# Kernel optimization log

Measured on AMD Instinct MI355X. Metric: run time of the kernel, lower is better.

The kernel has to match this reference:

```python
import jax, jax.numpy as jnp
import numpy as np

P, Q = 4, 16            # mlp_quad_last_shape
N, D_IN, H = 100000, 3, 256
N_QUAD = 128


def setup_inputs() -> dict:
    key = jax.random.key(0)
    ks = jax.random.split(key, 20)
    sc = lambda fan: 1.0 / np.sqrt(fan)
    inp = {}
    inp["input"] = jax.random.normal(ks[0], (N, D_IN), jnp.float32)
    inp["eq_param"] = jax.random.uniform(ks[1], (1,), jnp.float32)
    for i in range(5):
        inp[f"quad_x{i}"] = jax.random.uniform(ks[2 + i], (N_QUAD, 1), jnp.float32)
    # mlp_x params: Linear(3->256) -> tanh -> Linear(256->1024=P^5)
    inp["Wx1"] = jax.random.normal(ks[7], (D_IN, H), jnp.float32) * sc(D_IN)
    inp["bx1"] = jnp.zeros((H,), jnp.float32)
    inp["Wx2"] = jax.random.normal(ks[8], (H, P ** 5), jnp.float32) * sc(H)
    inp["bx2"] = jnp.zeros((P ** 5,), jnp.float32)
    # per-axis quad MLPs: Linear(1 -> P*Q)
    for i in range(5):
        inp[f"Wq{i}"] = jax.random.normal(ks[9 + i], (1, P * Q), jnp.float32) * sc(1)
        inp[f"bq{i}"] = jnp.zeros((P * Q,), jnp.float32)
    return inp


def reference(input, eq_param, quad_x0, quad_x1, quad_x2, quad_x3, quad_x4,
              Wx1, bx1, Wx2, bx2,
              Wq0, bq0, Wq1, bq1, Wq2, bq2, Wq3, bq3, Wq4, bq4):
    # lhs = mlp_x(input): [N, P^5]
    lhs = jnp.tanh(input @ Wx1 + bx1) @ Wx2 + bx2

    quads = (quad_x0, quad_x1, quad_x2, quad_x3, quad_x4)
    Ws = (Wq0, Wq1, Wq2, Wq3, Wq4)
    bs = (bq0, bq1, bq2, bq3, bq4)

    # Each factor: out_quad_i = y_i * (quad_x_i @ Wq_i + bq_i), reshape [n_i, P, Q].
    # The original einsum 'abx,cdx,efx,lmx,wvx->abcdeflmwv' followed by movedims,
    # reshape and sum over the merged n-axes is a multilinear map, so summing
    # each factor over its n_i axis FIRST gives the identical rhs tensor
    # (sum commutes with the outer product), avoiding the 10-D intermediate.
    ss = []
    for qx, W, b in zip(quads, Ws, bs):
        y = jnp.exp(-jnp.sum(qx * qx, axis=-1, keepdims=True) * eq_param[0])  # r_func weight [n_i,1]
        oq = (y * (qx @ W + b)).reshape(-1, P, Q)  # [n_i, P, Q]
        ss.append(jnp.sum(oq, axis=0))             # [P, Q]
    s0, s1, s2, s3, s4 = ss
    # rhs[b,d,f,m,v] = sum_x s0[b,x] s1[d,x] s2[f,x] s3[m,x] s4[v,x]  -> flatten to [P^5]
    rhs = jnp.einsum('bx,dx,fx,mx,vx->bdfmv', s0, s1, s2, s3, s4).reshape(-1)
    return lhs @ rhs  # [N]
```

## Files before the change

kernel.cpp:

```cpp
#include <hip/hip_runtime.h>

#define PP 4
#define QQ 16
#define NQ 128
#define HH 256
#define P5 1024

__device__ __forceinline__ float block_sum256(float v, float* red, int t) {
#pragma unroll
  for (int o = 32; o > 0; o >>= 1) v += __shfl_down(v, o, 64);
  if ((t & 63) == 0) red[t >> 6] = v;
  __syncthreads();
  float r = red[0] + red[1] + red[2] + red[3];
  __syncthreads();
  return r;
}

__global__ __launch_bounds__(256) void prep_kernel(
    const float* __restrict__ eq,
    const float* __restrict__ q0, const float* __restrict__ q1,
    const float* __restrict__ q2, const float* __restrict__ q3,
    const float* __restrict__ q4,
    const float* __restrict__ Wx1, const float* __restrict__ bx1,
    const float* __restrict__ Wx2, const float* __restrict__ bx2,
    const float* __restrict__ Wq0, const float* __restrict__ bq0,
    const float* __restrict__ Wq1, const float* __restrict__ bq1,
    const float* __restrict__ Wq2, const float* __restrict__ bq2,
    const float* __restrict__ Wq3, const float* __restrict__ bq3,
    const float* __restrict__ Wq4, const float* __restrict__ bq4,
    float* __restrict__ ws) {
  __shared__ float red[4];
  __shared__ float sS[5][64];
  __shared__ float sRhs[P5];

  const int t = threadIdx.x;
  const int hb = blockIdx.x;
  const float eqv = eq[0];

  const float* qs[5]  = {q0, q1, q2, q3, q4};
  const float* Wqs[5] = {Wq0, Wq1, Wq2, Wq3, Wq4};
  const float* bqs[5] = {bq0, bq1, bq2, bq3, bq4};

  float A[5], B[5];
#pragma unroll
  for (int i = 0; i < 5; ++i) {
    float a = 0.f, b = 0.f;
    if (t < NQ) {
      float x = qs[i][t];
      float y = expf(-x * x * eqv);
      a = y * x;
      b = y;
    }
    A[i] = block_sum256(a, red, t);
    B[i] = block_sum256(b, red, t);
  }

  for (int k = t; k < 5 * 64; k += 256) {
    int i = k >> 6, j = k & 63;
    sS[i][j] = Wqs[i][j] * A[i] + bqs[i][j] * B[i];
  }
  __syncthreads();

  for (int idx = t; idx < P5; idx += 256) {
    int b = (idx >> 8) & 3, d = (idx >> 6) & 3, f = (idx >> 4) & 3,
        m = (idx >> 2) & 3, v = idx & 3;
    float s = 0.f;
#pragma unroll
    for (int x = 0; x < QQ; ++x)
      s += sS[0][b * QQ + x] * sS[1][d * QQ + x] * sS[2][f * QQ + x] *
           sS[3][m * QQ + x] * sS[4][v * QQ + x];
    sRhs[idx] = s;
  }
  __syncthreads();

  const float* wrow = Wx2 + hb * P5;
  float p = 0.f;
#pragma unroll
  for (int k = 0; k < 4; ++k)
    p = fmaf(wrow[t + 256 * k], sRhs[t + 256 * k], p);
  p = block_sum256(p, red, t);
  if (t == 0) ws[hb * 8 + 4] = p;

  if (hb == 0) {
    if (t < HH) {
      ws[t * 8 + 0] = Wx1[t];
      ws[t * 8 + 1] = Wx1[HH + t];
      ws[t * 8 + 2] = Wx1[2 * HH + t];
      ws[t * 8 + 3] = bx1[t];
    }
    float pb = 0.f;
    for (int j = t; j < P5; j += 256) pb = fmaf(bx2[j], sRhs[j], pb);
    pb = block_sum256(pb, red, t);
    if (t == 0) ws[HH * 8] = pb;
  }
}

__global__ __launch_bounds__(256) void main_kernel(
    const float* __restrict__ input, const float* __restrict__ pk,
    float* __restrict__ out, int n) {
  __shared__ float sacc[4][64];
  const int lane = threadIdx.x & 63;
  const int wv   = threadIdx.x >> 6;
  const int row  = blockIdx.x * 64 + lane;
  const bool valid = row < n;

  float x0 = 0.f, x1 = 0.f, x2 = 0.f;
  if (valid) {
    x0 = input[row * 3 + 0];
    x1 = input[row * 3 + 1];
    x2 = input[row * 3 + 2];
  }

  const float* __restrict__ p = pk + wv * 64 * 8;
  float acc = 0.f;
#pragma unroll 8
  for (int h = 0; h < 64; ++h) {
    const float w0 = p[h * 8 + 0];
    const float w1 = p[h * 8 + 1];
    const float w2 = p[h * 8 + 2];
    const float b  = p[h * 8 + 3];
    const float wr = p[h * 8 + 4];
    float a = fmaf(x2, w2, fmaf(x1, w1, fmaf(x0, w0, b)));
    float ex = __expf(2.0f * a);
    float tnh = fmaf(-2.0f, __builtin_amdgcn_rcpf(ex + 1.0f), 1.0f);
    acc = fmaf(tnh, wr, acc);
  }
  sacc[wv][lane] = acc;
  __syncthreads();

  if (wv == 0 && valid) {
    float r = sacc[0][lane] + sacc[1][lane] + sacc[2][lane] + sacc[3][lane];
    out[row] = r + pk[HH * 8];
  }
}

extern "C" void kernel_launch(void* const* d_in, const int* in_sizes, int n_in,
                              void* d_out, int out_size, void* d_ws,
                              size_t ws_size, hipStream_t stream) {
  const float* input = (const float*)d_in[0];
  const float* eq    = (const float*)d_in[1];
  const float* q0    = (const float*)d_in[2];
  const float* q1    = (const float*)d_in[3];
  const float* q2    = (const float*)d_in[4];
  const float* q3    = (const float*)d_in[5];
  const float* q4    = (const float*)d_in[6];
  const float* Wx1   = (const float*)d_in[7];
  const float* bx1   = (const float*)d_in[8];
  const float* Wx2   = (const float*)d_in[9];
  const float* bx2   = (const float*)d_in[10];
  const float* Wq0   = (const float*)d_in[11];
  const float* bq0   = (const float*)d_in[12];
  const float* Wq1   = (const float*)d_in[13];
  const float* bq1   = (const float*)d_in[14];
  const float* Wq2   = (const float*)d_in[15];
  const float* bq2   = (const float*)d_in[16];
  const float* Wq3   = (const float*)d_in[17];
  const float* bq3   = (const float*)d_in[18];
  const float* Wq4   = (const float*)d_in[19];
  const float* bq4   = (const float*)d_in[20];

  float* ws  = (float*)d_ws;
  float* out = (float*)d_out;
  const int n = in_sizes[0] / 3;

  hipLaunchKernelGGL(prep_kernel, dim3(HH), dim3(256), 0, stream,
                     eq, q0, q1, q2, q3, q4, Wx1, bx1, Wx2, bx2,
                     Wq0, bq0, Wq1, bq1, Wq2, bq2, Wq3, bq3, Wq4, bq4, ws);

  const int blocks = (n + 63) / 64;
  hipLaunchKernelGGL(main_kernel, dim3(blocks), dim3(256), 0, stream,
                     input, ws, out, n);
}
```

Before: 118.9 us.

## Give each thread all hidden units and drop cross-wave LDS reduction

The main kernel now launches one-wave blocks where each thread loops over all 256 hidden units with four independent accumulators. This replaces the four-wave split of the hidden dimension, which needed a shared-memory reduction and a barrier. It removes LDS traffic and synchronization. In exchange it cuts the number of resident waves by four, which reduces latency hiding and worsens tail balance across CUs.

```diff
diff --git a/kernel.cpp b/kernel.cpp
--- a/kernel.cpp
+++ b/kernel.cpp
@@ -87,6 +87,9 @@
       ws[t * 8 + 1] = Wx1[HH + t];
       ws[t * 8 + 2] = Wx1[2 * HH + t];
       ws[t * 8 + 3] = bx1[t];
+      ws[t * 8 + 5] = 0.f;
+      ws[t * 8 + 6] = 0.f;
+      ws[t * 8 + 7] = 0.f;
     }
     float pb = 0.f;
     for (int j = t; j < P5; j += 256) pb = fmaf(bx2[j], sRhs[j], pb);
@@ -95,13 +98,10 @@
   }
 }
 
-__global__ __launch_bounds__(256) void main_kernel(
+__global__ __launch_bounds__(64) void main_kernel(
     const float* __restrict__ input, const float* __restrict__ pk,
     float* __restrict__ out, int n) {
-  __shared__ float sacc[4][64];
-  const int lane = threadIdx.x & 63;
-  const int wv   = threadIdx.x >> 6;
-  const int row  = blockIdx.x * 64 + lane;
+  const int row = blockIdx.x * 64 + threadIdx.x;
   const bool valid = row < n;
 
   float x0 = 0.f, x1 = 0.f, x2 = 0.f;
@@ -111,27 +111,27 @@
     x2 = input[row * 3 + 2];
   }
 
-  const float* __restrict__ p = pk + wv * 64 * 8;
-  float acc = 0.f;
+  float acc0 = 0.f, acc1 = 0.f, acc2 = 0.f, acc3 = 0.f;
 #pragma unroll 8
-  for (int h = 0; h < 64; ++h) {
-    const float w0 = p[h * 8 + 0];
-    const float w1 = p[h * 8 + 1];
-    const float w2 = p[h * 8 + 2];
-    const float b  = p[h * 8 + 3];
-    const float wr = p[h * 8 + 4];
-    float a = fmaf(x2, w2, fmaf(x1, w1, fmaf(x0, w0, b)));
-    float ex = __expf(2.0f * a);
-    float tnh = fmaf(-2.0f, __builtin_amdgcn_rcpf(ex + 1.0f), 1.0f);
-    acc = fmaf(tnh, wr, acc);
+  for (int h = 0; h < HH; h += 4) {
+#pragma unroll
+    for (int u = 0; u < 4; ++u) {
+      const float w0 = pk[(h + u) * 8 + 0];
+      const float w1 = pk[(h + u) * 8 + 1];
+      const float w2 = pk[(h + u) * 8 + 2];
+      const float b  = pk[(h + u) * 8 + 3];
+      const float wr = pk[(h + u) * 8 + 4];
+      float a = fmaf(x2, w2, fmaf(x1, w1, fmaf(x0, w0, b)));
+      float ex = __expf(2.0f * a);
+      float tnh = fmaf(-2.0f, __builtin_amdgcn_rcpf(ex + 1.0f), 1.0f);
+      if (u == 0) acc0 = fmaf(tnh, wr, acc0);
+      else if (u == 1) acc1 = fmaf(tnh, wr, acc1);
+      else if (u == 2) acc2 = fmaf(tnh, wr, acc2);
+      else acc3 = fmaf(tnh, wr, acc3);
+    }
   }
-  sacc[wv][lane] = acc;
-  __syncthreads();
 
-  if (wv == 0 && valid) {
-    float r = sacc[0][lane] + sacc[1][lane] + sacc[2][lane] + sacc[3][lane];
-    out[row] = r + pk[HH * 8];
-  }
+  if (valid) out[row] = (acc0 + acc1) + (acc2 + acc3) + pk[HH * 8];
 }
 
 extern "C" void kernel_launch(void* const* d_in, const int* in_sizes, int n_in,
@@ -168,6 +168,6 @@
                      Wq0, bq0, Wq1, bq1, Wq2, bq2, Wq3, bq3, Wq4, bq4, ws);
 
   const int blocks = (n + 63) / 64;
-  hipLaunchKernelGGL(main_kernel, dim3(blocks), dim3(256), 0, stream,
+  hipLaunchKernelGGL(main_kernel, dim3(blocks), dim3(64), 0, stream,
                      input, ws, out, n);
 }
```

Measured after the change: 142.1 us. 19.6% more time.

## Restructure main kernel: per-thread rows over full hidden dim with folded tanh constants

Applied to the files above, without the earlier changes.

The main kernel now assigns two rows per thread across all 256 hidden units, with no split across wavefronts or shared-memory reduction. Weights are staged in LDS as float4 tables with the 2*log2(e) scale pre-folded, so each unit needs only exp2 and rcp. Tanh is rewritten as 1 - 2/(e+1), with the constant sum of the output weights folded into a single bias. The prep kernel batches its ten block reductions and uses exp2f. Each block redoes the small table setup and reduction, and the grid has fewer, larger blocks.

```diff
diff --git a/kernel.cpp b/kernel.cpp
--- a/kernel.cpp
+++ b/kernel.cpp
@@ -1,10 +1,11 @@
 #include <hip/hip_runtime.h>
 
-#define PP 4
 #define QQ 16
 #define NQ 128
 #define HH 256
 #define P5 1024
+#define LOG2E   1.44269504088896340f
+#define K2LOG2E 2.88539008177792681f
 
 __device__ __forceinline__ float block_sum256(float v, float* red, int t) {
 #pragma unroll
@@ -21,7 +22,6 @@
     const float* __restrict__ q0, const float* __restrict__ q1,
     const float* __restrict__ q2, const float* __restrict__ q3,
     const float* __restrict__ q4,
-    const float* __restrict__ Wx1, const float* __restrict__ bx1,
     const float* __restrict__ Wx2, const float* __restrict__ bx2,
     const float* __restrict__ Wq0, const float* __restrict__ bq0,
     const float* __restrict__ Wq1, const float* __restrict__ bq1,
@@ -29,46 +29,58 @@
     const float* __restrict__ Wq3, const float* __restrict__ bq3,
     const float* __restrict__ Wq4, const float* __restrict__ bq4,
     float* __restrict__ ws) {
-  __shared__ float red[4];
   __shared__ float sS[5][64];
   __shared__ float sRhs[P5];
+  __shared__ float sPart[4][10];
+  __shared__ float sAB[10];
+  __shared__ float red[4];
 
   const int t = threadIdx.x;
   const int hb = blockIdx.x;
-  const float eqv = eq[0];
+  const float c = -eq[0] * LOG2E;
 
   const float* qs[5]  = {q0, q1, q2, q3, q4};
   const float* Wqs[5] = {Wq0, Wq1, Wq2, Wq3, Wq4};
   const float* bqs[5] = {bq0, bq1, bq2, bq3, bq4};
 
-  float A[5], B[5];
+  float v[10];
 #pragma unroll
   for (int i = 0; i < 5; ++i) {
     float a = 0.f, b = 0.f;
     if (t < NQ) {
       float x = qs[i][t];
-      float y = expf(-x * x * eqv);
+      float y = exp2f(x * x * c);
       a = y * x;
       b = y;
     }
-    A[i] = block_sum256(a, red, t);
-    B[i] = block_sum256(b, red, t);
+    v[2 * i] = a;
+    v[2 * i + 1] = b;
   }
+#pragma unroll
+  for (int k = 0; k < 10; ++k) {
+    float s = v[k];
+#pragma unroll
+    for (int o = 32; o > 0; o >>= 1) s += __shfl_down(s, o, 64);
+    if ((t & 63) == 0) sPart[t >> 6][k] = s;
+  }
+  __syncthreads();
+  if (t < 10) sAB[t] = sPart[0][t] + sPart[1][t] + sPart[2][t] + sPart[3][t];
+  __syncthreads();
 
   for (int k = t; k < 5 * 64; k += 256) {
     int i = k >> 6, j = k & 63;
-    sS[i][j] = Wqs[i][j] * A[i] + bqs[i][j] * B[i];
+    sS[i][j] = Wqs[i][j] * sAB[2 * i] + bqs[i][j] * sAB[2 * i + 1];
   }
   __syncthreads();
 
   for (int idx = t; idx < P5; idx += 256) {
     int b = (idx >> 8) & 3, d = (idx >> 6) & 3, f = (idx >> 4) & 3,
-        m = (idx >> 2) & 3, v = idx & 3;
+        m = (idx >> 2) & 3, w = idx & 3;
     float s = 0.f;
 #pragma unroll
     for (int x = 0; x < QQ; ++x)
       s += sS[0][b * QQ + x] * sS[1][d * QQ + x] * sS[2][f * QQ + x] *
-           sS[3][m * QQ + x] * sS[4][v * QQ + x];
+           sS[3][m * QQ + x] * sS[4][w * QQ + x];
     sRhs[idx] = s;
   }
   __syncthreads();
@@ -79,59 +91,67 @@
   for (int k = 0; k < 4; ++k)
     p = fmaf(wrow[t + 256 * k], sRhs[t + 256 * k], p);
   p = block_sum256(p, red, t);
-  if (t == 0) ws[hb * 8 + 4] = p;
+  if (t == 0) ws[hb] = p;
 
   if (hb == 0) {
-    if (t < HH) {
-      ws[t * 8 + 0] = Wx1[t];
-      ws[t * 8 + 1] = Wx1[HH + t];
-      ws[t * 8 + 2] = Wx1[2 * HH + t];
-      ws[t * 8 + 3] = bx1[t];
-    }
     float pb = 0.f;
     for (int j = t; j < P5; j += 256) pb = fmaf(bx2[j], sRhs[j], pb);
     pb = block_sum256(pb, red, t);
-    if (t == 0) ws[HH * 8] = pb;
+    if (t == 0) ws[HH] = pb;
   }
 }
 
 __global__ __launch_bounds__(256) void main_kernel(
-    const float* __restrict__ input, const float* __restrict__ pk,
+    const float* __restrict__ input, const float* __restrict__ Wx1,
+    const float* __restrict__ bx1, const float* __restrict__ wsv,
     float* __restrict__ out, int n) {
-  __shared__ float sacc[4][64];
-  const int lane = threadIdx.x & 63;
-  const int wv   = threadIdx.x >> 6;
-  const int row  = blockIdx.x * 64 + lane;
-  const bool valid = row < n;
+  __shared__ float4 qtab[HH];
+  __shared__ float4 wtabv[HH / 4];
+  __shared__ float red[4];
 
-  float x0 = 0.f, x1 = 0.f, x2 = 0.f;
-  if (valid) {
-    x0 = input[row * 3 + 0];
-    x1 = input[row * 3 + 1];
-    x2 = input[row * 3 + 2];
+  const int t = threadIdx.x;
+
+  float w2r = wsv[t];
+  qtab[t] = make_float4(K2LOG2E * Wx1[t], K2LOG2E * Wx1[HH + t],
+                        K2LOG2E * Wx1[2 * HH + t], K2LOG2E * bx1[t]);
+  ((float*)wtabv)[t] = -2.0f * w2r;
+
+  float s = w2r;
+#pragma unroll
+  for (int o = 32; o > 0; o >>= 1) s += __shfl_down(s, o, 64);
+  if ((t & 63) == 0) red[t >> 6] = s;
+  __syncthreads();
+  const float CONST = red[0] + red[1] + red[2] + red[3] + wsv[HH];
+
+  const int rA = blockIdx.x * 512 + t;
+  const int rB = rA + 256;
+  const bool vA = rA < n, vB = rB < n;
+  float xa0 = 0.f, xa1 = 0.f, xa2 = 0.f;
+  float xb0 = 0.f, xb1 = 0.f, xb2 = 0.f;
+  if (vA) { xa0 = input[rA * 3]; xa1 = input[rA * 3 + 1]; xa2 = input[rA * 3 + 2]; }
+  if (vB) { xb0 = input[rB * 3]; xb1 = input[rB * 3 + 1]; xb2 = input[rB * 3 + 2]; }
+
+  float accA = 0.f, accB = 0.f;
+#pragma unroll 4
+  for (int h4 = 0; h4 < HH / 4; ++h4) {
+    const float4 wq = wtabv[h4];
+    const float wrv[4] = {wq.x, wq.y, wq.z, wq.w};
+#pragma unroll
+    for (int u = 0; u < 4; ++u) {
+      const float4 q = qtab[h4 * 4 + u];
+      float aA = fmaf(q.z, xa2, fmaf(q.y, xa1, fmaf(q.x, xa0, q.w)));
+      float aB = fmaf(q.z, xb2, fmaf(q.y, xb1, fmaf(q.x, xb0, q.w)));
+      float eA = exp2f(aA);
+      float eB = exp2f(aB);
+      float rA_ = __builtin_amdgcn_rcpf(eA + 1.0f);
+      float rB_ = __builtin_amdgcn_rcpf(eB + 1.0f);
+      accA = fmaf(wrv[u], rA_, accA);
+      accB = fmaf(wrv[u], rB_, accB);
+    }
   }
 
-  const float* __restrict__ p = pk + wv * 64 * 8;
-  float acc = 0.f;
-#pragma unroll 8
-  for (int h = 0; h < 64; ++h) {
-    const float w0 = p[h * 8 + 0];
-    const float w1 = p[h * 8 + 1];
-    const float w2 = p[h * 8 + 2];
-    const float b  = p[h * 8 + 3];
-    const float wr = p[h * 8 + 4];
-    float a = fmaf(x2, w2, fmaf(x1, w1, fmaf(x0, w0, b)));
-    float ex = __expf(2.0f * a);
-    float tnh = fmaf(-2.0f, __builtin_amdgcn_rcpf(ex + 1.0f), 1.0f);
-    acc = fmaf(tnh, wr, acc);
-  }
-  sacc[wv][lane] = acc;
-  __syncthreads();
-
-  if (wv == 0 && valid) {
-    float r = sacc[0][lane] + sacc[1][lane] + sacc[2][lane] + sacc[3][lane];
-    out[row] = r + pk[HH * 8];
-  }
+  if (vA) out[rA] = accA + CONST;
+  if (vB) out[rB] = accB + CONST;
 }
 
 extern "C" void kernel_launch(void* const* d_in, const int* in_sizes, int n_in,
@@ -164,10 +184,10 @@
   const int n = in_sizes[0] / 3;
 
   hipLaunchKernelGGL(prep_kernel, dim3(HH), dim3(256), 0, stream,
-                     eq, q0, q1, q2, q3, q4, Wx1, bx1, Wx2, bx2,
+                     eq, q0, q1, q2, q3, q4, Wx2, bx2,
                      Wq0, bq0, Wq1, bq1, Wq2, bq2, Wq3, bq3, Wq4, bq4, ws);
 
-  const int blocks = (n + 63) / 64;
+  const int blocks = (n + 511) / 512;
   hipLaunchKernelGGL(main_kernel, dim3(blocks), dim3(256), 0, stream,
-                     input, ws, out, n);
+                     input, Wx1, bx1, ws, out, n);
 }
```

New measurement: 119.6 us. About the same (+0.6%).
